# Optimization experiments

Hardware: AMD Instinct MI355X
Metric: run time of the kernel (lower is better)

Reference implementation:

```python
import jax, jax.numpy as jnp
import numpy as np

N_NODES = 100_000
N_EDGES = 500_000
G = 1024          # num_graphs
H = 128           # hidden_dim
S_PER = 4         # start nodes per graph
EPS_LN = 1e-5


def _ln(x, g, b):
    m = x.mean(-1, keepdims=True)
    v = ((x - m) ** 2).mean(-1, keepdims=True)
    return (x - m) / jnp.sqrt(v + EPS_LN) * g + b


def _gelu(x):
    return jax.nn.gelu(x, approximate=False)  # torch nn.GELU default (erf)


def setup_inputs() -> dict:
    key = jax.random.key(0)
    ks = jax.random.split(key, 24)
    S = G * S_PER
    d = {
        'node_tokens': jax.random.normal(ks[0], (N_NODES, H), jnp.float32),
        'question_tokens': jax.random.normal(ks[1], (G, H), jnp.float32),
        'edge_tokens': jax.random.normal(ks[2], (N_EDGES, H), jnp.float32),
        'start_node_locals': jax.random.randint(ks[3], (S,), 0, N_NODES),
        'start_node_ptr': jnp.arange(G + 1) * S_PER,
        'edge_batch': jnp.sort(jax.random.randint(ks[4], (N_EDGES,), 0, G)),
        'selected_mask': jax.random.bernoulli(ks[5], 0.5, (N_EDGES,)),
        'edge_index': jax.random.randint(ks[6], (2, N_EDGES), 0, N_NODES),
    }
    w = lambda k, shp: jax.random.normal(k, shp, jnp.float32) * 0.02
    # log_z_head: LN(H) -> Linear(H,H) -> GELU -> Linear(H,1)
    d['ln1_g'] = jnp.ones((H,)); d['ln1_b'] = jnp.zeros((H,))
    d['zw1'] = w(ks[7], (H, H)); d['zb1'] = w(ks[8], (H,))
    d['zw2'] = w(ks[9], (H, 1)); d['zb2'] = jnp.zeros((1,))
    # ctx_projector: Linear(2H,H) -> GELU -> Linear(H,H)
    d['cw1'] = w(ks[10], (2 * H, H)); d['cb1'] = w(ks[11], (H,))
    d['cw2'] = w(ks[12], (H, H)); d['cb2'] = w(ks[13], (H,))
    # backward_head: LN(3H) -> Linear(3H,H) -> GELU -> (Dropout: identity in eval) -> Linear(H,1)
    d['bln_g'] = jnp.ones((3 * H,)); d['bln_b'] = jnp.zeros((3 * H,))
    d['bw1'] = w(ks[14], (3 * H, H)); d['bb1'] = w(ks[15], (H,))
    d['bw2'] = w(ks[16], (H, 1)); d['bb2'] = jnp.zeros((1,))
    return d


def reference(node_tokens, question_tokens, edge_tokens,
              ln1_g, ln1_b, zw1, zb1, zw2, zb2,
              cw1, cb1, cw2, cb2,
              bln_g, bln_b, bw1, bb1, bw2, bb2,
              start_node_locals, start_node_ptr, edge_batch, selected_mask, edge_index):
    counts = start_node_ptr[1:] - start_node_ptr[:-1]                       # [G]
    batch_index = jnp.repeat(jnp.arange(G), counts, total_repeat_length=start_node_locals.shape[0])
    # --- aggregate_start: gather + segment softmax + scatter-add ---
    start_tokens = node_tokens[start_node_locals]                            # [S,H]
    q = question_tokens[batch_index]                                         # [S,H]
    scores = (start_tokens * q).sum(-1) / jnp.sqrt(jnp.float32(H))           # [S]
    m = jax.ops.segment_max(scores, batch_index, num_segments=G)             # [G]
    ex = jnp.exp(scores - m[batch_index])
    denom = jax.ops.segment_sum(ex, batch_index, num_segments=G)
    alpha = ex / denom[batch_index]                                          # pyg_softmax (eps-free path)
    summary = jax.ops.segment_sum(start_tokens * alpha[:, None], batch_index, num_segments=G)  # [G,H]
    # --- build_context + log_z ---
    ctx_in = jnp.concatenate([summary, question_tokens], axis=-1)            # [G,2H]
    context = _gelu(ctx_in @ cw1 + cb1) @ cw2 + cb2                          # [G,H]
    log_z = (_gelu(_ln(context, ln1_g, ln1_b) @ zw1 + zb1) @ zw2 + zb2)[:, 0]  # [G]
    # --- log_pb (learned): gather + segment log-softmax over target nodes + scatter-add per graph ---
    tgt = edge_index[1]                                                      # [E]
    tail = node_tokens[tgt]                                                  # [E,H]
    edge_ctx = jnp.concatenate([edge_tokens, question_tokens[edge_batch], tail], axis=-1)  # [E,3H]
    logits = (_gelu(_ln(edge_ctx, bln_g, bln_b) @ bw1 + bb1) @ bw2 + bb2)[:, 0]            # [E]
    tmax = jax.ops.segment_max(logits, tgt, num_segments=N_NODES)
    shifted = logits - tmax[tgt]
    lse = jnp.log(jax.ops.segment_sum(jnp.exp(shifted), tgt, num_segments=N_NODES))
    log_probs = shifted - lse[tgt]                                           # scatter_log_softmax
    sel = selected_mask.astype(logits.dtype)
    log_pb_per_graph = jax.ops.segment_sum(log_probs * sel, edge_batch, num_segments=G)    # [G]
    # pb_nll: masked mean over graphs that have a selected edge
    nll_per_graph = jax.ops.segment_sum(-log_probs * sel, edge_batch, num_segments=G)
    has_edge = jax.ops.segment_sum(sel, edge_batch, num_segments=G) > 0
    pb_nll = jnp.where(has_edge, nll_per_graph, 0.0).sum() / jnp.maximum(has_edge.sum(), 1).astype(logits.dtype)
    return jnp.stack([log_z, log_pb_per_graph, jnp.broadcast_to(pb_nll, log_z.shape)], axis=-1)  # [G,3]
```

## Files before the change

kernel.cpp:

```cpp
#include <hip/hip_runtime.h>
#include <math.h>

#define G_NUM 1024
#define H 128
#define NNODES 100000
#define NEDGES 500000
#define EPS_LN 1e-5f

typedef __attribute__((ext_vector_type(8))) short short8;
typedef __attribute__((ext_vector_type(4))) float f32x4;

__device__ __forceinline__ float gelu_exact(float x) {
    return 0.5f * x * (1.0f + erff(x * 0.70710678118654752440f));
}
__device__ __forceinline__ unsigned short f2bf(float x) {
    unsigned u = __float_as_uint(x);
    return (unsigned short)((u + 0x7FFFu + ((u >> 16) & 1u)) >> 16);
}

__global__ void k_probe_mask(const unsigned* __restrict__ mw, int* __restrict__ flag) {
    unsigned v = mw[threadIdx.x];
    if (v == 0x3F800000u) atomicOr(flag, 2);
    else if (v > 1u) atomicOr(flag, 1);
}

__global__ void k_prep(const float* __restrict__ bw1, const float* __restrict__ blng,
                       unsigned short* __restrict__ bwbf) {
    int e = blockIdx.x * 256 + threadIdx.x;
    if (e >= 384 * 128) return;
    int k = e >> 7, n = e & 127;
    int s = k >> 5, krel = k & 31;
    int quad = krel >> 3, j = krel & 7;
    int lane = quad * 16 + (n & 15);
    int t8 = n >> 4;
    bwbf[((s * 8 + t8) * 64 + lane) * 8 + j] = f2bf(bw1[e] * blng[k]);
}

__global__ __launch_bounds__(128) void k_prep2(const float* __restrict__ bw1,
                                               const float* __restrict__ blng,
                                               const float* __restrict__ blnb,
                                               const float* __restrict__ bb1,
                                               float* __restrict__ colsum,
                                               float* __restrict__ bb1p) {
    int n = threadIdx.x;
    float cs = 0.f, bs = 0.f;
    for (int k = 0; k < 384; ++k) {
        float w = bw1[k * H + n];
        cs += blng[k] * w;
        bs += blnb[k] * w;
    }
    colsum[n] = cs;
    bb1p[n] = bb1[n] + bs;
}

__global__ __launch_bounds__(128) void k_graph(
    const float* __restrict__ node_tokens, const float* __restrict__ question,
    const int* __restrict__ locals_, const int* __restrict__ ptr,
    const float* __restrict__ cw1, const float* __restrict__ cb1,
    const float* __restrict__ cw2, const float* __restrict__ cb2,
    const float* __restrict__ ln1g, const float* __restrict__ ln1b,
    const float* __restrict__ zw1, const float* __restrict__ zb1,
    const float* __restrict__ zw2, const float* __restrict__ zb2,
    float* __restrict__ out)
{
    int g = blockIdx.x, t = threadIdx.x;
    __shared__ float xin[2 * H];
    __shared__ float buf[H];
    __shared__ float r1[2], r2[2];
    __shared__ float sc[16];
    int p0 = ptr[g], p1 = ptr[g + 1];
    int cnt = p1 - p0; if (cnt > 16) cnt = 16;
    float q = question[(size_t)g * H + t];
    xin[H + t] = q;
    for (int s = 0; s < cnt; ++s) {
        int node = locals_[p0 + s];
        float v = node_tokens[(size_t)node * H + t] * q;
        for (int off = 32; off; off >>= 1) v += __shfl_down(v, off);
        if ((t & 63) == 0) r1[t >> 6] = v;
        __syncthreads();
        if (t == 0) sc[s] = (r1[0] + r1[1]) * 0.08838834764831845f;
        __syncthreads();
    }
    float m = -1e30f;
    for (int s = 0; s < cnt; ++s) m = fmaxf(m, sc[s]);
    float den = 0.f;
    for (int s = 0; s < cnt; ++s) den += expf(sc[s] - m);
    float acc0 = 0.f;
    for (int s = 0; s < cnt; ++s) {
        float a = expf(sc[s] - m) / den;
        acc0 += a * node_tokens[(size_t)locals_[p0 + s] * H + t];
    }
    xin[t] = acc0;
    __syncthreads();
    float a1 = cb1[t];
    for (int k = 0; k < 2 * H; ++k) a1 += xin[k] * cw1[k * H + t];
    buf[t] = gelu_exact(a1);
    __syncthreads();
    float ctx = cb2[t];
    for (int k = 0; k < H; ++k) ctx += buf[k] * cw2[k * H + t];
    float s1 = ctx, s2 = ctx * ctx;
    for (int off = 32; off; off >>= 1) { s1 += __shfl_down(s1, off); s2 += __shfl_down(s2, off); }
    if ((t & 63) == 0) { r1[t >> 6] = s1; r2[t >> 6] = s2; }
    __syncthreads();
    float mean = (r1[0] + r1[1]) * (1.f / H);
    float var  = (r2[0] + r2[1]) * (1.f / H) - mean * mean;
    float xn = (ctx - mean) * rsqrtf(var + EPS_LN) * ln1g[t] + ln1b[t];
    __syncthreads();
    buf[t] = xn;
    __syncthreads();
    float a2 = zb1[t];
    for (int k = 0; k < H; ++k) a2 += buf[k] * zw1[k * H + t];
    float p = gelu_exact(a2) * zw2[t];
    for (int off = 32; off; off >>= 1) p += __shfl_down(p, off);
    if ((t & 63) == 0) r1[t >> 6] = p;
    __syncthreads();
    if (t == 0) out[(size_t)g * 3 + 0] = r1[0] + r1[1] + zb2[0];
}

__global__ __launch_bounds__(256) void k_edges(
    const float* __restrict__ node_tokens, const float* __restrict__ question,
    const float* __restrict__ edge_tokens, const int* __restrict__ edge_batch,
    const int* __restrict__ edge_index,
    const unsigned short* __restrict__ bwbf, const float* __restrict__ colsum,
    const float* __restrict__ bb1p, const float* __restrict__ bw2,
    const float* __restrict__ bb2, float* __restrict__ logits,
    float* __restrict__ sumexp)
{
    __shared__ unsigned short bstage[4096];
    int t = threadIdx.x, lane = t & 63, w = t >> 6;
    int quad = lane >> 4, n16 = lane & 15;
    int e0 = blockIdx.x * 64;
    int e = e0 + w * 16 + n16;
    int ec = e < NEDGES ? e : NEDGES - 1;
    int qrow = edge_batch[ec];
    int trow = edge_index[NEDGES + ec];
    const float4* ep = (const float4*)(edge_tokens + (size_t)ec * H);
    const float4* qp = (const float4*)(question + (size_t)qrow * H);
    const float4* np_ = (const float4*)(node_tokens + (size_t)trow * H);

    float s1 = 0.f, s2 = 0.f;
    short8 frag[12];
    #pragma unroll
    for (int s = 0; s < 12; ++s) {
        int c0 = s * 8 + quad * 2;
        const float4* base = (s < 4) ? ep : (s < 8) ? qp : np_;
        int cc = c0 - ((s < 4) ? 0 : (s < 8) ? 32 : 64);
        float4 v0 = base[cc], v1 = base[cc + 1];
        s1 += v0.x + v0.y + v0.z + v0.w + v1.x + v1.y + v1.z + v1.w;
        s2 += v0.x*v0.x + v0.y*v0.y + v0.z*v0.z + v0.w*v0.w
            + v1.x*v1.x + v1.y*v1.y + v1.z*v1.z + v1.w*v1.w;
        short8 f;
        f[0] = (short)f2bf(v0.x); f[1] = (short)f2bf(v0.y);
        f[2] = (short)f2bf(v0.z); f[3] = (short)f2bf(v0.w);
        f[4] = (short)f2bf(v1.x); f[5] = (short)f2bf(v1.y);
        f[6] = (short)f2bf(v1.z); f[7] = (short)f2bf(v1.w);
        frag[s] = f;
    }
    s1 += __shfl_xor(s1, 16); s1 += __shfl_xor(s1, 32);
    s2 += __shfl_xor(s2, 16); s2 += __shfl_xor(s2, 32);
    float mu  = s1 * (1.f / 384.f);
    float inv = rsqrtf(s2 * (1.f / 384.f) - mu * mu + EPS_LN);

    f32x4 acc[8];
    #pragma unroll
    for (int q = 0; q < 8; ++q) acc[q] = (f32x4){0.f, 0.f, 0.f, 0.f};

    #pragma unroll
    for (int s = 0; s < 12; ++s) {
        __syncthreads();
        {
            const uint4* src = (const uint4*)(bwbf + s * 4096);
            uint4* dst = (uint4*)bstage;
            dst[t] = src[t];
            dst[t + 256] = src[t + 256];
        }
        __syncthreads();
        #pragma unroll
        for (int t8 = 0; t8 < 8; ++t8) {
            short8 b = *(const short8*)&bstage[(t8 * 64 + lane) * 8];
            acc[t8] = __builtin_amdgcn_mfma_f32_16x16x32_bf16(frag[s], b, acc[t8], 0, 0, 0);
        }
    }

    float csv[8], bbv[8], w2v[8];
    #pragma unroll
    for (int t8 = 0; t8 < 8; ++t8) {
        int n = t8 * 16 + n16;
        csv[t8] = colsum[n]; bbv[t8] = bb1p[n]; w2v[t8] = bw2[n];
    }
    float bb2v = bb2[0];
    #pragma unroll
    for (int r = 0; r < 4; ++r) {
        float mu_r  = __shfl(mu,  quad * 4 + r);
        float inv_r = __shfl(inv, quad * 4 + r);
        float ssum = 0.f;
        #pragma unroll
        for (int t8 = 0; t8 < 8; ++t8) {
            float y = (acc[t8][r] - mu_r * csv[t8]) * inv_r + bbv[t8];
            ssum += gelu_exact(y) * w2v[t8];
        }
        ssum += __shfl_xor(ssum, 1);
        ssum += __shfl_xor(ssum, 2);
        ssum += __shfl_xor(ssum, 4);
        ssum += __shfl_xor(ssum, 8);
        if (n16 == 0) {
            int ei = e0 + w * 16 + quad * 4 + r;
            if (ei < NEDGES) {
                float lg = ssum + bb2v;
                logits[ei] = lg;
                atomicAdd(&sumexp[edge_index[NEDGES + ei]], expf(lg));
            }
        }
    }
}

__global__ __launch_bounds__(256) void k_logpb(
    const float* __restrict__ logits,
    const int* __restrict__ edge_index,
    const int* __restrict__ edge_batch,
    const void* __restrict__ mask,
    const int* __restrict__ flag,
    const float* __restrict__ sumexp,
    float* __restrict__ logpb, int* __restrict__ selcnt)
{
    __shared__ float lacc[8];
    __shared__ int lcnt[8];
    __shared__ int g0s, big;
    int t = threadIdx.x;
    int e0 = blockIdx.x * 256;
    if (t == 0) {
        int ga = edge_batch[e0 < NEDGES ? e0 : NEDGES - 1];
        int el = e0 + 255; if (el >= NEDGES) el = NEDGES - 1;
        int gb = edge_batch[el];
        g0s = ga; big = (gb - ga > 7);
    }
    if (t < 8) { lacc[t] = 0.f; lcnt[t] = 0; }
    __syncthreads();
    int e = e0 + t;
    if (e < NEDGES) {
        int mode = *flag;
        bool sel;
        if (mode & 2)      sel = ((const float*)mask)[e] != 0.f;
        else if (mode & 1) sel = ((const unsigned char*)mask)[e] != 0;
        else               sel = ((const int*)mask)[e] != 0;
        if (sel) {
            int tg = edge_index[NEDGES + e];
            float lp = logits[e] - logf(sumexp[tg]);
            int g = edge_batch[e];
            if (!big) {
                atomicAdd(&lacc[g - g0s], lp);
                atomicAdd(&lcnt[g - g0s], 1);
            } else {
                atomicAdd(&logpb[g], lp);
                atomicAdd(&selcnt[g], 1);
            }
        }
    }
    __syncthreads();
    if (t < 8 && !big && lcnt[t] > 0) {
        atomicAdd(&logpb[g0s + t], lacc[t]);
        atomicAdd(&selcnt[g0s + t], lcnt[t]);
    }
}

__global__ __launch_bounds__(1024) void k_final(const float* __restrict__ logpb,
                                                const int* __restrict__ selcnt,
                                                float* __restrict__ out)
{
    int g = threadIdx.x;
    float lpb = logpb[g];
    int has = selcnt[g] > 0;
    float s = has ? -lpb : 0.f;
    int c = has;
    __shared__ float rn[16];
    __shared__ int rh[16];
    __shared__ float pbnll_s;
    for (int off = 32; off; off >>= 1) { s += __shfl_down(s, off); c += __shfl_down(c, off); }
    if ((g & 63) == 0) { rn[g >> 6] = s; rh[g >> 6] = c; }
    __syncthreads();
    if (g == 0) {
        float ts = 0.f; int tc = 0;
        for (int i = 0; i < 16; ++i) { ts += rn[i]; tc += rh[i]; }
        pbnll_s = ts / (float)(tc > 0 ? tc : 1);
    }
    __syncthreads();
    out[(size_t)g * 3 + 1] = lpb;
    out[(size_t)g * 3 + 2] = pbnll_s;
}

extern "C" void kernel_launch(void* const* d_in, const int* in_sizes, int n_in,
                              void* d_out, int out_size, void* d_ws, size_t ws_size,
                              hipStream_t stream) {
    const float* node_tokens = (const float*)d_in[0];
    const float* question    = (const float*)d_in[1];
    const float* edge_tokens = (const float*)d_in[2];
    const int*   locals_     = (const int*)d_in[3];
    const int*   ptr         = (const int*)d_in[4];
    const int*   edge_batch  = (const int*)d_in[5];
    const void*  mask        = d_in[6];
    const int*   edge_index  = (const int*)d_in[7];
    const float* ln1g = (const float*)d_in[8];
    const float* ln1b = (const float*)d_in[9];
    const float* zw1  = (const float*)d_in[10];
    const float* zb1  = (const float*)d_in[11];
    const float* zw2  = (const float*)d_in[12];
    const float* zb2  = (const float*)d_in[13];
    const float* cw1  = (const float*)d_in[14];
    const float* cb1  = (const float*)d_in[15];
    const float* cw2  = (const float*)d_in[16];
    const float* cb2  = (const float*)d_in[17];
    const float* blng = (const float*)d_in[18];
    const float* blnb = (const float*)d_in[19];
    const float* bw1  = (const float*)d_in[20];
    const float* bb1  = (const float*)d_in[21];
    const float* bw2  = (const float*)d_in[22];
    const float* bb2  = (const float*)d_in[23];
    float* out = (float*)d_out;

    float* ws = (float*)d_ws;
    float* sumexp  = ws;
    float* logpb   = ws + 100000;
    int*   selcnt  = (int*)(ws + 101024);
    int*   flag    = (int*)(ws + 102048);
    float* logits  = ws + 102052;
    float* colsum  = ws + 602052;
    float* bb1p    = ws + 602180;
    unsigned short* bwbf = (unsigned short*)(ws + 602308);

    hipMemsetAsync(d_ws, 0, (size_t)102049 * 4, stream);
    k_probe_mask<<<1, 256, 0, stream>>>((const unsigned*)mask, flag);
    k_prep<<<192, 256, 0, stream>>>(bw1, blng, bwbf);
    k_prep2<<<1, 128, 0, stream>>>(bw1, blng, blnb, bb1, colsum, bb1p);
    k_graph<<<G_NUM, 128, 0, stream>>>(node_tokens, question, locals_, ptr,
                                       cw1, cb1, cw2, cb2, ln1g, ln1b,
                                       zw1, zb1, zw2, zb2, out);
    k_edges<<<(NEDGES + 63) / 64, 256, 0, stream>>>(node_tokens, question, edge_tokens,
                                                    edge_batch, edge_index, bwbf,
                                                    colsum, bb1p, bw2, bb2,
                                                    logits, sumexp);
    int eb = (NEDGES + 255) / 256;
    k_logpb<<<eb, 256, 0, stream>>>(logits, edge_index, edge_batch, mask, flag,
                                    sumexp, logpb, selcnt);
    k_final<<<1, 1024, 0, stream>>>(logpb, selcnt, out);
}
```

Before: 621.5 us.

## Make k_edges persistent with full bf16 weight matrix resident in LDS

Rewrites the edge kernel as a persistent grid of 256 blocks of 1024 threads. Each block loads the whole 384x128 bf16 weight matrix (96KB) into LDS once, then loops over 256-edge tiles, so the 12 per-slice global-to-LDS restaging steps and their barriers per block go away. The cost is one LDS-heavy block per CU, which limits occupancy and latency hiding for the gathered activation loads. __launch_bounds__(1024, 4) may also constrain registers and cause spills.

```diff
diff --git a/kernel.cpp b/kernel.cpp
--- a/kernel.cpp
+++ b/kernel.cpp
@@ -117,7 +117,7 @@
     if (t == 0) out[(size_t)g * 3 + 0] = r1[0] + r1[1] + zb2[0];
 }
 
-__global__ __launch_bounds__(256) void k_edges(
+__global__ __launch_bounds__(1024, 4) void k_edges(
     const float* __restrict__ node_tokens, const float* __restrict__ question,
     const float* __restrict__ edge_tokens, const int* __restrict__ edge_batch,
     const int* __restrict__ edge_index,
@@ -126,62 +126,16 @@
     const float* __restrict__ bb2, float* __restrict__ logits,
     float* __restrict__ sumexp)
 {
-    __shared__ unsigned short bstage[4096];
+    __shared__ unsigned short bwlds[49152];
     int t = threadIdx.x, lane = t & 63, w = t >> 6;
     int quad = lane >> 4, n16 = lane & 15;
-    int e0 = blockIdx.x * 64;
-    int e = e0 + w * 16 + n16;
-    int ec = e < NEDGES ? e : NEDGES - 1;
-    int qrow = edge_batch[ec];
-    int trow = edge_index[NEDGES + ec];
-    const float4* ep = (const float4*)(edge_tokens + (size_t)ec * H);
-    const float4* qp = (const float4*)(question + (size_t)qrow * H);
-    const float4* np_ = (const float4*)(node_tokens + (size_t)trow * H);
-
-    float s1 = 0.f, s2 = 0.f;
-    short8 frag[12];
-    #pragma unroll
-    for (int s = 0; s < 12; ++s) {
-        int c0 = s * 8 + quad * 2;
-        const float4* base = (s < 4) ? ep : (s < 8) ? qp : np_;
-        int cc = c0 - ((s < 4) ? 0 : (s < 8) ? 32 : 64);
-        float4 v0 = base[cc], v1 = base[cc + 1];
-        s1 += v0.x + v0.y + v0.z + v0.w + v1.x + v1.y + v1.z + v1.w;
-        s2 += v0.x*v0.x + v0.y*v0.y + v0.z*v0.z + v0.w*v0.w
-            + v1.x*v1.x + v1.y*v1.y + v1.z*v1.z + v1.w*v1.w;
-        short8 f;
-        f[0] = (short)f2bf(v0.x); f[1] = (short)f2bf(v0.y);
-        f[2] = (short)f2bf(v0.z); f[3] = (short)f2bf(v0.w);
-        f[4] = (short)f2bf(v1.x); f[5] = (short)f2bf(v1.y);
-        f[6] = (short)f2bf(v1.z); f[7] = (short)f2bf(v1.w);
-        frag[s] = f;
-    }
-    s1 += __shfl_xor(s1, 16); s1 += __shfl_xor(s1, 32);
-    s2 += __shfl_xor(s2, 16); s2 += __shfl_xor(s2, 32);
-    float mu  = s1 * (1.f / 384.f);
-    float inv = rsqrtf(s2 * (1.f / 384.f) - mu * mu + EPS_LN);
-
-    f32x4 acc[8];
-    #pragma unroll
-    for (int q = 0; q < 8; ++q) acc[q] = (f32x4){0.f, 0.f, 0.f, 0.f};
-
-    #pragma unroll
-    for (int s = 0; s < 12; ++s) {
-        __syncthreads();
-        {
-            const uint4* src = (const uint4*)(bwbf + s * 4096);
-            uint4* dst = (uint4*)bstage;
-            dst[t] = src[t];
-            dst[t + 256] = src[t + 256];
-        }
-        __syncthreads();
-        #pragma unroll
-        for (int t8 = 0; t8 < 8; ++t8) {
-            short8 b = *(const short8*)&bstage[(t8 * 64 + lane) * 8];
-            acc[t8] = __builtin_amdgcn_mfma_f32_16x16x32_bf16(frag[s], b, acc[t8], 0, 0, 0);
-        }
-    }
-
+
+    {
+        const uint4* src = (const uint4*)bwbf;
+        uint4* dst = (uint4*)bwlds;
+        #pragma unroll
+        for (int i = 0; i < 6; ++i) dst[t + i * 1024] = src[t + i * 1024];
+    }
     float csv[8], bbv[8], w2v[8];
     #pragma unroll
     for (int t8 = 0; t8 < 8; ++t8) {
@@ -189,26 +143,77 @@
         csv[t8] = colsum[n]; bbv[t8] = bb1p[n]; w2v[t8] = bw2[n];
     }
     float bb2v = bb2[0];
-    #pragma unroll
-    for (int r = 0; r < 4; ++r) {
-        float mu_r  = __shfl(mu,  quad * 4 + r);
-        float inv_r = __shfl(inv, quad * 4 + r);
-        float ssum = 0.f;
-        #pragma unroll
-        for (int t8 = 0; t8 < 8; ++t8) {
-            float y = (acc[t8][r] - mu_r * csv[t8]) * inv_r + bbv[t8];
-            ssum += gelu_exact(y) * w2v[t8];
+    const int* tgt_idx = edge_index + NEDGES;
+    __syncthreads();
+
+    const int NTILES = (NEDGES + 255) / 256;
+    for (int tile = blockIdx.x; tile < NTILES; tile += gridDim.x) {
+        int e0w = tile * 256 + w * 16;
+        int e = e0w + n16;
+        int ec = e < NEDGES ? e : NEDGES - 1;
+        int qrow = edge_batch[ec];
+        int trow = tgt_idx[ec];
+        const float4* ep  = (const float4*)(edge_tokens + (size_t)ec * H);
+        const float4* qp  = (const float4*)(question + (size_t)qrow * H);
+        const float4* np_ = (const float4*)(node_tokens + (size_t)trow * H);
+
+        float s1 = 0.f, s2 = 0.f;
+        short8 frag[12];
+        #pragma unroll
+        for (int s = 0; s < 12; ++s) {
+            int c0 = s * 8 + quad * 2;
+            const float4* base = (s < 4) ? ep : (s < 8) ? qp : np_;
+            int cc = c0 - ((s < 4) ? 0 : (s < 8) ? 32 : 64);
+            float4 v0 = base[cc], v1 = base[cc + 1];
+            s1 += v0.x + v0.y + v0.z + v0.w + v1.x + v1.y + v1.z + v1.w;
+            s2 += v0.x*v0.x + v0.y*v0.y + v0.z*v0.z + v0.w*v0.w
+                + v1.x*v1.x + v1.y*v1.y + v1.z*v1.z + v1.w*v1.w;
+            short8 f;
+            f[0] = (short)f2bf(v0.x); f[1] = (short)f2bf(v0.y);
+            f[2] = (short)f2bf(v0.z); f[3] = (short)f2bf(v0.w);
+            f[4] = (short)f2bf(v1.x); f[5] = (short)f2bf(v1.y);
+            f[6] = (short)f2bf(v1.z); f[7] = (short)f2bf(v1.w);
+            frag[s] = f;
         }
-        ssum += __shfl_xor(ssum, 1);
-        ssum += __shfl_xor(ssum, 2);
-        ssum += __shfl_xor(ssum, 4);
-        ssum += __shfl_xor(ssum, 8);
-        if (n16 == 0) {
-            int ei = e0 + w * 16 + quad * 4 + r;
-            if (ei < NEDGES) {
-                float lg = ssum + bb2v;
-                logits[ei] = lg;
-                atomicAdd(&sumexp[edge_index[NEDGES + ei]], expf(lg));
+        s1 += __shfl_xor(s1, 16); s1 += __shfl_xor(s1, 32);
+        s2 += __shfl_xor(s2, 16); s2 += __shfl_xor(s2, 32);
+        float mu  = s1 * (1.f / 384.f);
+        float inv = rsqrtf(s2 * (1.f / 384.f) - mu * mu + EPS_LN);
+
+        f32x4 acc[8];
+        #pragma unroll
+        for (int q = 0; q < 8; ++q) acc[q] = (f32x4){0.f, 0.f, 0.f, 0.f};
+
+        #pragma unroll
+        for (int s = 0; s < 12; ++s) {
+            #pragma unroll
+            for (int t8 = 0; t8 < 8; ++t8) {
+                short8 b = *(const short8*)&bwlds[((s * 8 + t8) * 64 + lane) * 8];
+                acc[t8] = __builtin_amdgcn_mfma_f32_16x16x32_bf16(frag[s], b, acc[t8], 0, 0, 0);
+            }
+        }
+
+        #pragma unroll
+        for (int r = 0; r < 4; ++r) {
+            float mu_r  = __shfl(mu,  quad * 4 + r);
+            float inv_r = __shfl(inv, quad * 4 + r);
+            float ssum = 0.f;
+            #pragma unroll
+            for (int t8 = 0; t8 < 8; ++t8) {
+                float y = (acc[t8][r] - mu_r * csv[t8]) * inv_r + bbv[t8];
+                ssum += gelu_exact(y) * w2v[t8];
+            }
+            ssum += __shfl_xor(ssum, 1);
+            ssum += __shfl_xor(ssum, 2);
+            ssum += __shfl_xor(ssum, 4);
+            ssum += __shfl_xor(ssum, 8);
+            if (n16 == 0) {
+                int ei = e0w + quad * 4 + r;
+                if (ei < NEDGES) {
+                    float lg = ssum + bb2v;
+                    logits[ei] = lg;
+                    atomicAdd(&sumexp[tgt_idx[ei]], expf(lg));
+                }
             }
         }
     }
@@ -334,10 +339,10 @@
     k_graph<<<G_NUM, 128, 0, stream>>>(node_tokens, question, locals_, ptr,
                                        cw1, cb1, cw2, cb2, ln1g, ln1b,
                                        zw1, zb1, zw2, zb2, out);
-    k_edges<<<(NEDGES + 63) / 64, 256, 0, stream>>>(node_tokens, question, edge_tokens,
-                                                    edge_batch, edge_index, bwbf,
-                                                    colsum, bb1p, bw2, bb2,
-                                                    logits, sumexp);
+    k_edges<<<256, 1024, 0, stream>>>(node_tokens, question, edge_tokens,
+                                      edge_batch, edge_index, bwbf,
+                                      colsum, bb1p, bw2, bb2,
+                                      logits, sumexp);
     int eb = (NEDGES + 255) / 256;
     k_logpb<<<eb, 256, 0, stream>>>(logits, edge_index, edge_batch, mask, flag,
                                     sumexp, logpb, selcnt);
```

Result: slower. 1.291 ms (+107.8%).

## Split edge scoring into LayerNorm-pack and MFMA GEMM passes over workspace chunks

Applied to the files above, without the earlier changes.

Merges the three prep kernels into one launch. When workspace allows, replaces the fused edge kernel with two chunked passes. The first gathers rows, applies LayerNorm and writes bf16 fragments in MFMA layout. The second streams them through a double-buffered weight GEMM that adds GELU, the output dot and the logsumexp atomics. This aims to decouple the irregular gathers from the matrix math, at the cost of an extra round trip of about 384 MB of bf16 through memory and more launches.

```diff
diff --git a/kernel.cpp b/kernel.cpp
--- a/kernel.cpp
+++ b/kernel.cpp
@@ -18,39 +18,47 @@
     return (unsigned short)((u + 0x7FFFu + ((u >> 16) & 1u)) >> 16);
 }
 
-__global__ void k_probe_mask(const unsigned* __restrict__ mw, int* __restrict__ flag) {
-    unsigned v = mw[threadIdx.x];
-    if (v == 0x3F800000u) atomicOr(flag, 2);
-    else if (v > 1u) atomicOr(flag, 1);
-}
-
-__global__ void k_prep(const float* __restrict__ bw1, const float* __restrict__ blng,
-                       unsigned short* __restrict__ bwbf) {
-    int e = blockIdx.x * 256 + threadIdx.x;
-    if (e >= 384 * 128) return;
-    int k = e >> 7, n = e & 127;
-    int s = k >> 5, krel = k & 31;
-    int quad = krel >> 3, j = krel & 7;
-    int lane = quad * 16 + (n & 15);
-    int t8 = n >> 4;
-    bwbf[((s * 8 + t8) * 64 + lane) * 8 + j] = f2bf(bw1[e] * blng[k]);
-}
-
-__global__ __launch_bounds__(128) void k_prep2(const float* __restrict__ bw1,
-                                               const float* __restrict__ blng,
-                                               const float* __restrict__ blnb,
-                                               const float* __restrict__ bb1,
-                                               float* __restrict__ colsum,
-                                               float* __restrict__ bb1p) {
-    int n = threadIdx.x;
-    float cs = 0.f, bs = 0.f;
-    for (int k = 0; k < 384; ++k) {
-        float w = bw1[k * H + n];
-        cs += blng[k] * w;
-        bs += blnb[k] * w;
-    }
-    colsum[n] = cs;
-    bb1p[n] = bb1[n] + bs;
+__global__ __launch_bounds__(256) void k_prep_all(
+    const float* __restrict__ bw1, const float* __restrict__ blng,
+    const float* __restrict__ blnb, const float* __restrict__ bb1,
+    unsigned short* __restrict__ bwbf, float* __restrict__ colsum,
+    float* __restrict__ bb1p,
+    const unsigned* __restrict__ mw, int* __restrict__ flag, int fold)
+{
+    __shared__ float rc[4], rb[4];
+    int b = blockIdx.x, t = threadIdx.x;
+    if (b < 192) {
+        int e = b * 256 + t;
+        int k = e >> 7, n = e & 127;
+        int s = k >> 5, krel = k & 31;
+        int quad = krel >> 3, j = krel & 7;
+        int lane = quad * 16 + (n & 15);
+        int t8 = n >> 4;
+        float m = fold ? blng[k] : 1.0f;
+        bwbf[((s * 8 + t8) * 64 + lane) * 8 + j] = f2bf(bw1[e] * m);
+    } else if (b < 320) {
+        int n = b - 192;
+        float cs = 0.f, bs = 0.f;
+        for (int k = t; k < 384; k += 256) {
+            float w = bw1[k * H + n];
+            cs += blng[k] * w;
+            bs += blnb[k] * w;
+        }
+        for (int off = 32; off; off >>= 1) {
+            cs += __shfl_down(cs, off);
+            bs += __shfl_down(bs, off);
+        }
+        if ((t & 63) == 0) { rc[t >> 6] = cs; rb[t >> 6] = bs; }
+        __syncthreads();
+        if (t == 0) {
+            colsum[n] = rc[0] + rc[1] + rc[2] + rc[3];
+            bb1p[n]   = bb1[n] + rb[0] + rb[1] + rb[2] + rb[3];
+        }
+    } else {
+        unsigned v = mw[t];
+        if (v == 0x3F800000u) atomicOr(flag, 2);
+        else if (v > 1u) atomicOr(flag, 1);
+    }
 }
 
 __global__ __launch_bounds__(128) void k_graph(
@@ -115,6 +123,144 @@
     if ((t & 63) == 0) r1[t >> 6] = p;
     __syncthreads();
     if (t == 0) out[(size_t)g * 3 + 0] = r1[0] + r1[1] + zb2[0];
+}
+
+__global__ __launch_bounds__(256) void k_pack(
+    const float* __restrict__ node_tokens, const float* __restrict__ question,
+    const float* __restrict__ edge_tokens, const int* __restrict__ edge_batch,
+    const int* __restrict__ edge_index,
+    const float* __restrict__ blng, const float* __restrict__ blnb,
+    unsigned short* __restrict__ apk, int e_base)
+{
+    __shared__ float ssm[4][16], ssq[4][16];
+    int t = threadIdx.x, lane = t & 63, w = t >> 6;
+    int quad = lane >> 4, n16 = lane & 15;
+    int e = e_base + blockIdx.x * 16 + n16;
+    int ec = e < NEDGES ? e : NEDGES - 1;
+    int qrow = edge_batch[ec];
+    int trow = edge_index[NEDGES + ec];
+    const float4* ep = (const float4*)(edge_tokens + (size_t)ec * H);
+    const float4* qp = (const float4*)(question + (size_t)qrow * H);
+    const float4* np = (const float4*)(node_tokens + (size_t)trow * H);
+
+    float4 d0a, d0b, d1a, d1b, d2a, d2b;
+    float ps = 0.f, pq = 0.f;
+    #pragma unroll
+    for (int i = 0; i < 3; ++i) {
+        int s = w * 3 + i;
+        int c0 = s * 8 + quad * 2;
+        int cc = c0 - ((s < 4) ? 0 : (s < 8) ? 32 : 64);
+        const float4* base = (s < 4) ? ep : (s < 8) ? qp : np;
+        float4 v0 = base[cc], v1 = base[cc + 1];
+        if (i == 0) { d0a = v0; d0b = v1; }
+        else if (i == 1) { d1a = v0; d1b = v1; }
+        else { d2a = v0; d2b = v1; }
+        ps += v0.x + v0.y + v0.z + v0.w + v1.x + v1.y + v1.z + v1.w;
+        pq += v0.x*v0.x + v0.y*v0.y + v0.z*v0.z + v0.w*v0.w
+            + v1.x*v1.x + v1.y*v1.y + v1.z*v1.z + v1.w*v1.w;
+    }
+    ps += __shfl_xor(ps, 16); ps += __shfl_xor(ps, 32);
+    pq += __shfl_xor(pq, 16); pq += __shfl_xor(pq, 32);
+    if (quad == 0) { ssm[w][n16] = ps; ssq[w][n16] = pq; }
+    __syncthreads();
+    float S = ssm[0][n16] + ssm[1][n16] + ssm[2][n16] + ssm[3][n16];
+    float Q = ssq[0][n16] + ssq[1][n16] + ssq[2][n16] + ssq[3][n16];
+    float mu  = S * (1.f / 384.f);
+    float inv = rsqrtf(Q * (1.f / 384.f) - mu * mu + EPS_LN);
+
+    #pragma unroll
+    for (int i = 0; i < 3; ++i) {
+        int s = w * 3 + i;
+        int k0 = s * 32 + quad * 8;
+        float4 g0 = *(const float4*)(blng + k0), g1 = *(const float4*)(blng + k0 + 4);
+        float4 b0 = *(const float4*)(blnb + k0), b1 = *(const float4*)(blnb + k0 + 4);
+        float4 va = (i == 0) ? d0a : (i == 1) ? d1a : d2a;
+        float4 vb = (i == 0) ? d0b : (i == 1) ? d1b : d2b;
+        short8 f;
+        f[0] = (short)f2bf((va.x - mu) * inv * g0.x + b0.x);
+        f[1] = (short)f2bf((va.y - mu) * inv * g0.y + b0.y);
+        f[2] = (short)f2bf((va.z - mu) * inv * g0.z + b0.z);
+        f[3] = (short)f2bf((va.w - mu) * inv * g0.w + b0.w);
+        f[4] = (short)f2bf((vb.x - mu) * inv * g1.x + b1.x);
+        f[5] = (short)f2bf((vb.y - mu) * inv * g1.y + b1.y);
+        f[6] = (short)f2bf((vb.z - mu) * inv * g1.z + b1.z);
+        f[7] = (short)f2bf((vb.w - mu) * inv * g1.w + b1.w);
+        *(short8*)&apk[(((size_t)blockIdx.x * 12 + s) * 64 + lane) * 8] = f;
+    }
+}
+
+__global__ __launch_bounds__(256) void k_gemm(
+    const unsigned short* __restrict__ apk,
+    const unsigned short* __restrict__ bwbf,
+    const float* __restrict__ bb1, const float* __restrict__ bw2,
+    const float* __restrict__ bb2, const int* __restrict__ edge_index,
+    float* __restrict__ logits, float* __restrict__ sumexp,
+    int e_base, int e_cnt)
+{
+    __shared__ unsigned short bstage[2][4096];
+    int t = threadIdx.x, lane = t & 63, w = t >> 6;
+    int quad = lane >> 4, n16 = lane & 15;
+    const int* tgt_idx = edge_index + NEDGES;
+    int T = blockIdx.x * 4 + w;
+
+    {
+        const uint4* src = (const uint4*)bwbf;
+        uint4 a = src[t], b = src[t + 256];
+        uint4* dst = (uint4*)bstage[0];
+        dst[t] = a; dst[t + 256] = b;
+    }
+    __syncthreads();
+
+    f32x4 acc[8];
+    #pragma unroll
+    for (int i = 0; i < 8; ++i) acc[i] = (f32x4){0.f, 0.f, 0.f, 0.f};
+    const short8* afrag = (const short8*)apk + (size_t)T * 12 * 64;
+
+    #pragma unroll
+    for (int s = 0; s < 12; ++s) {
+        int cur = s & 1;
+        uint4 p0, p1;
+        if (s < 11) {
+            const uint4* src = (const uint4*)(bwbf + (s + 1) * 4096);
+            p0 = src[t]; p1 = src[t + 256];
+        }
+        short8 fa = afrag[s * 64 + lane];
+        #pragma unroll
+        for (int t8 = 0; t8 < 8; ++t8) {
+            short8 b = *(const short8*)&bstage[cur][(t8 * 64 + lane) * 8];
+            acc[t8] = __builtin_amdgcn_mfma_f32_16x16x32_bf16(fa, b, acc[t8], 0, 0, 0);
+        }
+        if (s < 11) {
+            uint4* dst = (uint4*)bstage[cur ^ 1];
+            dst[t] = p0; dst[t + 256] = p1;
+            __syncthreads();
+        }
+    }
+
+    float bb2v = bb2[0];
+    #pragma unroll
+    for (int r = 0; r < 4; ++r) {
+        float ssum = 0.f;
+        #pragma unroll
+        for (int t8 = 0; t8 < 8; ++t8) {
+            int n = t8 * 16 + n16;
+            float y = acc[t8][r] + bb1[n];
+            ssum += gelu_exact(y) * bw2[n];
+        }
+        ssum += __shfl_xor(ssum, 1);
+        ssum += __shfl_xor(ssum, 2);
+        ssum += __shfl_xor(ssum, 4);
+        ssum += __shfl_xor(ssum, 8);
+        if (n16 == 0) {
+            int elocal = T * 16 + quad * 4 + r;
+            int ei = e_base + elocal;
+            if (elocal < e_cnt && ei < NEDGES) {
+                float lg = ssum + bb2v;
+                logits[ei] = lg;
+                atomicAdd(&sumexp[tgt_idx[ei]], expf(lg));
+            }
+        }
+    }
 }
 
 __global__ __launch_bounds__(256) void k_edges(
@@ -326,18 +472,42 @@
     float* colsum  = ws + 602052;
     float* bb1p    = ws + 602180;
     unsigned short* bwbf = (unsigned short*)(ws + 602308);
+    const size_t base_floats = 626884;
+    unsigned short* apk = (unsigned short*)(ws + base_floats);
+
+    int CH = 0;
+    if (ws_size > base_floats * 4) {
+        size_t cap = (ws_size - base_floats * 4) / 768;
+        if      (cap >= 131072) CH = 131072;
+        else if (cap >= 65536)  CH = 65536;
+        else if (cap >= 32768)  CH = 32768;
+        else if (cap >= 16384)  CH = 16384;
+    }
 
     hipMemsetAsync(d_ws, 0, (size_t)102049 * 4, stream);
-    k_probe_mask<<<1, 256, 0, stream>>>((const unsigned*)mask, flag);
-    k_prep<<<192, 256, 0, stream>>>(bw1, blng, bwbf);
-    k_prep2<<<1, 128, 0, stream>>>(bw1, blng, blnb, bb1, colsum, bb1p);
+    k_prep_all<<<321, 256, 0, stream>>>(bw1, blng, blnb, bb1, bwbf, colsum, bb1p,
+                                        (const unsigned*)mask, flag, CH ? 0 : 1);
     k_graph<<<G_NUM, 128, 0, stream>>>(node_tokens, question, locals_, ptr,
                                        cw1, cb1, cw2, cb2, ln1g, ln1b,
                                        zw1, zb1, zw2, zb2, out);
-    k_edges<<<(NEDGES + 63) / 64, 256, 0, stream>>>(node_tokens, question, edge_tokens,
-                                                    edge_batch, edge_index, bwbf,
-                                                    colsum, bb1p, bw2, bb2,
-                                                    logits, sumexp);
+    if (CH) {
+        for (int e0 = 0; e0 < NEDGES; e0 += CH) {
+            int cnt = NEDGES - e0 < CH ? NEDGES - e0 : CH;
+            k_pack<<<(cnt + 15) / 16, 256, 0, stream>>>(node_tokens, question,
+                                                        edge_tokens, edge_batch,
+                                                        edge_index, blng, blnb,
+                                                        apk, e0);
+            k_gemm<<<(cnt + 63) / 64, 256, 0, stream>>>(apk, bwbf, bb1, bw2, bb2,
+                                                        edge_index, logits, sumexp,
+                                                        e0, cnt);
+        }
+    } else {
+        k_edges<<<(NEDGES + 63) / 64, 256, 0, stream>>>(node_tokens, question,
+                                                        edge_tokens, edge_batch,
+                                                        edge_index, bwbf, colsum,
+                                                        bb1p, bw2, bb2,
+                                                        logits, sumexp);
+    }
     int eb = (NEDGES + 255) / 256;
     k_logpb<<<eb, 256, 0, stream>>>(logits, edge_index, edge_batch, mask, flag,
                                     sumexp, logpb, selcnt);
```

After: 672.0 us. 1.08x slower.
